# Optimization experiments

Hardware: AMD Instinct MI355X
Metric: run time of the kernel (lower is better)

The kernel has to match this reference:

```python
import jax, jax.numpy as jnp
import numpy as np
import math

N_EMBD = 768
N_HEAD = 12
B, T, S = 8, 1024, 257
HEAD_DIM = N_EMBD // N_HEAD


def _ln(x, g, b, eps=1e-5):
    m = jnp.mean(x, axis=-1, keepdims=True)
    v = jnp.mean(jnp.square(x - m), axis=-1, keepdims=True)
    return (x - m) * jax.lax.rsqrt(v + eps) * g + b


def _heads(t, n_head):
    b, s, c = t.shape
    return t.reshape(b, s, n_head, c // n_head).transpose(0, 2, 1, 3)  # (B,H,S,D)


def setup_inputs() -> dict:
    key = jax.random.key(0)
    ks = jax.random.split(key, 12)
    sc = 0.02
    d, h4 = N_EMBD, 4 * N_EMBD
    return {
        "x": jax.random.normal(ks[0], (B, T, d), jnp.float32),
        "encoder_x": jax.random.normal(ks[1], (B, S, d), jnp.float32),
        "ln1_g": jnp.ones((d,), jnp.float32), "ln1_b": jnp.zeros((d,), jnp.float32),
        "ln2_g": jnp.ones((d,), jnp.float32), "ln2_b": jnp.zeros((d,), jnp.float32),
        "ln3_g": jnp.ones((d,), jnp.float32), "ln3_b": jnp.zeros((d,), jnp.float32),
        "attn_w": jax.random.normal(ks[2], (d, 3 * d), jnp.float32) * sc,
        "attn_b": jnp.zeros((3 * d,), jnp.float32),
        "attn_proj_w": jax.random.normal(ks[3], (d, d), jnp.float32) * sc,
        "attn_proj_b": jnp.zeros((d,), jnp.float32),
        "cross_w": jax.random.normal(ks[4], (d, 3 * d), jnp.float32) * sc,
        "cross_b": jnp.zeros((3 * d,), jnp.float32),
        "cross_proj_w": jax.random.normal(ks[5], (d, d), jnp.float32) * sc,
        "cross_proj_b": jnp.zeros((d,), jnp.float32),
        "fc_w": jax.random.normal(ks[6], (d, h4), jnp.float32) * sc,
        "fc_b": jnp.zeros((h4,), jnp.float32),
        "proj_w": jax.random.normal(ks[7], (h4, d), jnp.float32) * sc,
        "proj_b": jnp.zeros((d,), jnp.float32),
    }


def reference(x, encoder_x, ln1_g, ln1_b, ln2_g, ln2_b, ln3_g, ln3_b,
              attn_w, attn_b, attn_proj_w, attn_proj_b,
              cross_w, cross_b, cross_proj_w, cross_proj_b,
              fc_w, fc_b, proj_w, proj_b):
    d = N_EMBD
    scale = 1.0 / math.sqrt(HEAD_DIM)

    # --- causal self-attention ---
    h = _ln(x, ln1_g, ln1_b)
    qkv = h @ attn_w + attn_b
    q, k, v = (_heads(t, N_HEAD) for t in jnp.split(qkv, 3, axis=-1))
    att = jnp.einsum('bhqd,bhkd->bhqk', q, k) * scale
    t = x.shape[1]
    causal = jnp.tril(jnp.ones((t, t), bool))
    att = jnp.where(causal[None, None], att, -jnp.inf)
    att = jax.nn.softmax(att, axis=-1)
    o = jnp.einsum('bhqk,bhkd->bhqd', att, v)
    o = o.transpose(0, 2, 1, 3).reshape(x.shape)
    x = x + o @ attn_proj_w + attn_proj_b

    # --- cross-attention (shared c_attn for q from x, k/v from encoder) ---
    h = _ln(x, ln2_g, ln2_b)
    q = _heads((h @ cross_w + cross_b)[..., :d], N_HEAD)
    ekv = encoder_x @ cross_w + cross_b
    k = _heads(ekv[..., d:2 * d], N_HEAD)
    v = _heads(ekv[..., 2 * d:], N_HEAD)
    att = jax.nn.softmax(jnp.einsum('bhqd,bhkd->bhqk', q, k) * scale, axis=-1)
    o = jnp.einsum('bhqk,bhkd->bhqd', att, v)
    o = o.transpose(0, 2, 1, 3).reshape(x.shape)
    x = x + o @ cross_proj_w + cross_proj_b

    # --- MLP (GELU tanh) ---
    h = _ln(x, ln3_g, ln3_b)
    h = jax.nn.gelu(h @ fc_w + fc_b, approximate=True)
    x = x + h @ proj_w + proj_b
    return x
```

## Files before the change

### kernel.cpp

```cpp
#include <hip/hip_runtime.h>

typedef __bf16 bf16x8 __attribute__((ext_vector_type(8)));
typedef float  f32x4  __attribute__((ext_vector_type(4)));
typedef unsigned short u16;

#define N_EMBD 768
#define T_LEN 1024
#define S_LEN 257
#define S_PAD 320
#define BATCH 8
#define NH 12
#define BH (BATCH*NH)
#define HD 64

__device__ __forceinline__ u16 f2b(float f){
  union{float f; unsigned u;} v; v.f=f;
  unsigned r=(v.u + 0x7fffu + ((v.u>>16)&1u))>>16;
  return (u16)r;
}
__device__ __forceinline__ float b2f(u16 h){
  union{unsigned u; float f;} v; v.u=((unsigned)h)<<16;
  return v.f;
}
__device__ __forceinline__ void gl_lds16(const void* g, void* l){
  __builtin_amdgcn_global_load_lds((const __attribute__((address_space(1))) void*)g,
                                   (__attribute__((address_space(3))) void*)l, 16, 0, 0);
}

template<int C> __device__ __forceinline__ float dpp_mov_f(float x){
  union{float f;int i;} u; u.f=x;
  u.i = __builtin_amdgcn_mov_dpp(u.i, C, 0xf, 0xf, true);
  return u.f;
}
__device__ __forceinline__ float red16_add(float x){
  x = x + dpp_mov_f<0xB1>(x);
  x = x + dpp_mov_f<0x4E>(x);
  x = x + dpp_mov_f<0x141>(x);
  x = x + dpp_mov_f<0x140>(x);
  return x;
}

__global__ void prep_all(const float* __restrict__ s0,const float* __restrict__ s1,
                         const float* __restrict__ s2,const float* __restrict__ s3,
                         const float* __restrict__ s4,const float* __restrict__ s5,
                         u16* __restrict__ d0,u16* __restrict__ d1,
                         u16* __restrict__ d2,u16* __restrict__ d3,
                         u16* __restrict__ d4,u16* __restrict__ d5,
                         const float* __restrict__ enc, u16* __restrict__ enc_bf,
                         const float* __restrict__ xin, const float* __restrict__ g1,
                         const float* __restrict__ b1, u16* __restrict__ hbuf){
  __shared__ u16 tile[64][68];
  int id=blockIdx.x;
  if(id>=3846){
    int row  = (id-3846)*4 + (threadIdx.x>>6);
    int lane = threadIdx.x&63;
    size_t base = (size_t)row*N_EMBD;
    float v[12];
#pragma unroll
    for(int p=0;p<3;p++){
      int col = p*256 + lane*4;
      float4 f = *(const float4*)&xin[base+col];
      v[p*4]=f.x; v[p*4+1]=f.y; v[p*4+2]=f.z; v[p*4+3]=f.w;
    }
    float s=0.f, s2=0.f;
#pragma unroll
    for(int i=0;i<12;i++){ s+=v[i]; s2+=v[i]*v[i]; }
#pragma unroll
    for(int off=1; off<64; off<<=1){ s += __shfl_xor(s,off); s2 += __shfl_xor(s2,off); }
    float mean = s*(1.f/N_EMBD);
    float var  = s2*(1.f/N_EMBD) - mean*mean;
    float rstd = rsqrtf(var + 1e-5f);
#pragma unroll
    for(int p=0;p<3;p++){
      int col = p*256 + lane*4;
#pragma unroll
      for(int j=0;j<4;j++){
        hbuf[base+col+j] = f2b((v[p*4+j]-mean)*rstd*g1[col+j] + b1[col+j]);
      }
    }
    return;
  }
  if(id>=2304){
    int i = (id-2304)*256 + threadIdx.x;
    float4 f = *(const float4*)&enc[i*4];
    ushort4 u; u.x=f2b(f.x); u.y=f2b(f.y); u.z=f2b(f.z); u.w=f2b(f.w);
    *(ushort4*)&enc_bf[i*4] = u;
    return;
  }
  const float* in; u16* out; int K,N,t;
  if(id<432)      {in=s0;out=d0;K=768;N=2304;t=id;}
  else if(id<864) {in=s1;out=d1;K=768;N=2304;t=id-432;}
  else if(id<1008){in=s2;out=d2;K=768;N=768;t=id-864;}
  else if(id<1152){in=s3;out=d3;K=768;N=768;t=id-1008;}
  else if(id<1728){in=s4;out=d4;K=768;N=3072;t=id-1152;}
  else            {in=s5;out=d5;K=3072;N=768;t=id-1728;}
  int tiles_n=N>>6;
  int k0=(t/tiles_n)<<6, n0=(t%tiles_n)<<6;
  int tr = threadIdx.x>>4;
  int tc = (threadIdx.x&15)*4;
#pragma unroll
  for(int i=0;i<4;i++){
    float4 f = *(const float4*)&in[(size_t)(k0+tr+i*16)*N + n0 + tc];
    tile[tr+i*16][tc+0]=f2b(f.x); tile[tr+i*16][tc+1]=f2b(f.y);
    tile[tr+i*16][tc+2]=f2b(f.z); tile[tr+i*16][tc+3]=f2b(f.w);
  }
  __syncthreads();
#pragma unroll
  for(int i=0;i<4;i++){
    int n = n0+tr+i*16;
    ushort4 u;
    u.x=tile[tc+0][tr+i*16]; u.y=tile[tc+1][tr+i*16];
    u.z=tile[tc+2][tr+i*16]; u.w=tile[tc+3][tr+i*16];
    *(ushort4*)&out[(size_t)n*K + k0 + tc] = u;
  }
}

__global__ void ln_kernel(const float* __restrict__ x, const float* __restrict__ g,
                          const float* __restrict__ bta, u16* __restrict__ out){
  int row  = blockIdx.x*4 + (threadIdx.x>>6);
  int lane = threadIdx.x&63;
  size_t base = (size_t)row*N_EMBD;
  float v[12];
#pragma unroll
  for(int p=0;p<3;p++){
    int col = p*256 + lane*4;
    float4 f = *(const float4*)&x[base+col];
    v[p*4]=f.x; v[p*4+1]=f.y; v[p*4+2]=f.z; v[p*4+3]=f.w;
  }
  float s=0.f, s2=0.f;
#pragma unroll
  for(int i=0;i<12;i++){ s+=v[i]; s2+=v[i]*v[i]; }
#pragma unroll
  for(int off=1; off<64; off<<=1){ s += __shfl_xor(s,off); s2 += __shfl_xor(s2,off); }
  float mean = s*(1.f/N_EMBD);
  float var  = s2*(1.f/N_EMBD) - mean*mean;
  float rstd = rsqrtf(var + 1e-5f);
#pragma unroll
  for(int p=0;p<3;p++){
    int col = p*256 + lane*4;
#pragma unroll
    for(int j=0;j<4;j++){
      out[base+col+j] = f2b((v[p*4+j]-mean)*rstd*g[col+j] + bta[col+j]);
    }
  }
}

enum { M_QKV_SELF=0, M_Q_CROSS=1, M_KV_CROSS=2, M_RESID_F32=3,
       M_RESID_INPLACE=4, M_GELU=5, M_RESID_OUT=6 };

template<int MODE, int BN>
__global__ void gemm_bt(const u16* __restrict__ A, const u16* __restrict__ Wt,
                        const float* __restrict__ bias,
                        void* out0, void* out1, void* out2, const void* resid,
                        int M, int K, int Ntiles){
  constexpr int MI = (BN==128)?4:2;
  __shared__ u16 As[128*64];
  __shared__ u16 Bs[BN*64];
  int tid=threadIdx.x, wave=tid>>6, lane=tid&63;

  int Mtl = gridDim.x / Ntiles;
  int mt, nt;
  if((Mtl&7)==0){
    int xcd=blockIdx.x&7, j=blockIdx.x>>3, bpx=Mtl>>3;
    int band=j/Ntiles; nt=j-band*Ntiles; mt=xcd*bpx+band;
  } else { mt=blockIdx.x/Ntiles; nt=blockIdx.x-mt*Ntiles; }
  int m0=mt*128, n0=nt*BN;

  int wm = (BN==128)? (wave>>1)*64 : wave*32;
  int wn = (BN==128)? (wave&1)*64  : 0;
  int lrow=lane&15, quad=lane>>4;
  f32x4 acc[MI][4];
  f32x4 z = {0.f,0.f,0.f,0.f};
#pragma unroll
  for(int i=0;i<MI;i++)
#pragma unroll
    for(int j=0;j<4;j++) acc[i][j]=z;

  int srow  = wave*8 + (lane>>3);
  int c_src = (lane&7) ^ ((lane>>3)&7);
  int pa = quad ^ (lrow&7);

  const u16* ap[4];
#pragma unroll
  for(int i=0;i<4;i++){
    int ga = min(m0 + i*32 + srow, M-1);
    ap[i] = A + (size_t)ga*K + c_src*8;
  }
  const u16* bp[BN/32];
#pragma unroll
  for(int i=0;i<BN/32;i++)
    bp[i] = Wt + (size_t)(n0 + i*32 + srow)*K + c_src*8;

  for(int k0=0;k0<K;k0+=64){
#pragma unroll
    for(int i=0;i<4;i++)
      gl_lds16(ap[i] + k0, &As[(i*32+wave*8)*64]);
#pragma unroll
    for(int i=0;i<BN/32;i++)
      gl_lds16(bp[i] + k0, &Bs[(i*32+wave*8)*64]);
    __syncthreads();
    bf16x8 af[MI][2], bfr[4][2];
#pragma unroll
    for(int i=0;i<MI;i++){
      const u16* ab=&As[(wm+i*16+lrow)*64];
      af[i][0]=*(const bf16x8*)(ab+pa*8);
      af[i][1]=*(const bf16x8*)(ab+(pa^4)*8);
    }
#pragma unroll
    for(int i=0;i<4;i++){
      const u16* bb=&Bs[(wn+i*16+lrow)*64];
      bfr[i][0]=*(const bf16x8*)(bb+pa*8);
      bfr[i][1]=*(const bf16x8*)(bb+(pa^4)*8);
    }
#pragma unroll
    for(int h=0;h<2;h++)
#pragma unroll
      for(int mi=0;mi<MI;mi++)
#pragma unroll
        for(int ni=0;ni<4;ni++)
          acc[mi][ni] = __builtin_amdgcn_mfma_f32_16x16x32_bf16(af[mi][h], bfr[ni][h], acc[mi][ni], 0,0,0);
    __syncthreads();
  }

#pragma unroll
  for(int ni=0;ni<4;ni++){
    int n = n0 + wn + ni*16 + lrow;
    float bv = bias[n];
#pragma unroll
    for(int mi=0;mi<MI;mi++){
      int mbase = m0 + wm + mi*16 + quad*4;
      float cr[4];
#pragma unroll
      for(int r=0;r<4;r++) cr[r]=acc[mi][ni][r]+bv;

      if constexpr (MODE==M_QKV_SELF){
        int part=n/768, nn=n-part*768;
        int hh=nn>>6, dd=nn&63;
        int b=mbase>>10, t0=mbase&1023;
        size_t bh=(size_t)(b*NH+hh);
        if(part==0){
#pragma unroll
          for(int r=0;r<4;r++) ((u16*)out0)[(bh*T_LEN+t0+r)*HD+dd]=f2b(cr[r]*0.125f);
        } else if(part==1){
#pragma unroll
          for(int r=0;r<4;r++) ((u16*)out1)[(bh*T_LEN+t0+r)*HD+dd]=f2b(cr[r]);
        } else {
          ushort4 pk; pk.x=f2b(cr[0]); pk.y=f2b(cr[1]); pk.z=f2b(cr[2]); pk.w=f2b(cr[3]);
          *(ushort4*)&((u16*)out2)[(bh*HD+dd)*T_LEN+t0]=pk;
        }
      } else if constexpr (MODE==M_Q_CROSS){
        int b=mbase>>10, t0=mbase&1023;
        int hh=n>>6, dd=n&63;
        size_t bh=(size_t)(b*NH+hh);
#pragma unroll
        for(int r=0;r<4;r++) ((u16*)out0)[(bh*T_LEN+t0+r)*HD+dd]=f2b(cr[r]*0.125f);
      } else if constexpr (MODE==M_KV_CROSS){
        int part=n/768, nn=n-part*768;
        int hh=nn>>6, dd=nn&63;
#pragma unroll
        for(int r=0;r<4;r++){
          int m=mbase+r;
          if(m<M){
            int b=m/S_LEN, s=m-b*S_LEN;
            size_t bh=(size_t)(b*NH+hh);
            if(part==0) ((u16*)out0)[(bh*S_PAD+s)*HD+dd]=f2b(cr[r]);
            else        ((u16*)out1)[(bh*HD+dd)*S_PAD+s]=f2b(cr[r]);
          }
        }
      } else if constexpr (MODE==M_RESID_F32){
        const float* x=(const float*)resid;
#pragma unroll
        for(int r=0;r<4;r++){ int m=mbase+r;
          ((float*)out0)[(size_t)m*768+n]=x[(size_t)m*768+n]+cr[r]; }
      } else if constexpr (MODE==M_RESID_INPLACE){
#pragma unroll
        for(int r=0;r<4;r++){ int m=mbase+r;
          ((float*)out0)[(size_t)m*768+n]+=cr[r]; }
      } else if constexpr (MODE==M_GELU){
#pragma unroll
        for(int r=0;r<4;r++){
          int m=mbase+r;
          float uu=cr[r];
          float zz=0.7978845608028654f*(uu+0.044715f*uu*uu*uu);
          float t=__expf(2.f*zz);
          float th=1.f-2.f/(t+1.f);
          ((u16*)out0)[(size_t)m*3072+n]=f2b(0.5f*uu*(1.f+th));
        }
      } else {
        const float* x=(const float*)resid;
#pragma unroll
        for(int r=0;r<4;r++){ int m=mbase+r;
          ((float*)out0)[(size_t)m*768+n]=x[(size_t)m*768+n]+cr[r]; }
      }
    }
  }
}

template<bool CAUSAL>
__global__ __launch_bounds__(256,2)
void flash_attn(const u16* __restrict__ Q, const u16* __restrict__ Kk,
                const u16* __restrict__ V, u16* __restrict__ O,
                int Skey, int Spad){
  __shared__ u16 KT[2][64*64];
  __shared__ u16 VT[2][64*64];
  __shared__ u16 Plds[4][16][72];
  int bh = blockIdx.x % BH;
  int qbi= blockIdx.x / BH;
  int qb = CAUSAL ? (15-qbi) : qbi;
  int b=bh/NH, hh=bh-b*NH;
  int wave=threadIdx.x>>6, lane=threadIdx.x&63;
  int lrow=lane&15, quad=lane>>4;
  const u16* Qp=Q+(size_t)bh*T_LEN*HD;
  const u16* Kp=Kk+(size_t)bh*Spad*HD;
  const u16* Vp=V+(size_t)bh*HD*Spad;
  u16* Op=O+(size_t)b*T_LEN*N_EMBD+hh*HD;
  int q0 = qb*64 + wave*16;

  int r0    = wave*8 + (lane>>3);
  int c_src = (lane&7) ^ ((lane>>3)&7);

  bf16x8 aq0=*(const bf16x8*)&Qp[(size_t)(q0+lrow)*HD + quad*8];
  bf16x8 aq1=*(const bf16x8*)&Qp[(size_t)(q0+lrow)*HD + 32 + quad*8];

  f32x4 oacc[4];
  f32x4 z={0.f,0.f,0.f,0.f};
#pragma unroll
  for(int i=0;i<4;i++) oacc[i]=z;
  float lsum[4]={0.f,0.f,0.f,0.f};

  int nt = CAUSAL ? (qb+1) : ((Skey+63)>>6);

  {
    gl_lds16(Kp + (size_t)r0*HD        + c_src*8, &KT[0][(wave*8)*64]);
    gl_lds16(Kp + (size_t)(r0+32)*HD   + c_src*8, &KT[0][(32+wave*8)*64]);
    gl_lds16(Vp + (size_t)r0*Spad      + c_src*8, &VT[0][(wave*8)*64]);
    gl_lds16(Vp + (size_t)(r0+32)*Spad + c_src*8, &VT[0][(32+wave*8)*64]);
  }
  __syncthreads();

  int p0 = quad ^ (lrow&7);

  for(int it=0; it<nt; it++){
    int bb = it&1;
    int kt = it*64;
    if(it+1<nt){
      int ktn=(it+1)*64;
      gl_lds16(Kp + (size_t)(ktn+r0)*HD      + c_src*8, &KT[bb^1][(wave*8)*64]);
      gl_lds16(Kp + (size_t)(ktn+r0+32)*HD   + c_src*8, &KT[bb^1][(32+wave*8)*64]);
      gl_lds16(Vp + (size_t)r0*Spad      + ktn + c_src*8, &VT[bb^1][(wave*8)*64]);
      gl_lds16(Vp + (size_t)(r0+32)*Spad + ktn + c_src*8, &VT[bb^1][(32+wave*8)*64]);
    }
    f32x4 s[4];
#pragma unroll
    for(int g=0;g<4;g++){
      const u16* kb=&KT[bb][(g*16+lrow)*64];
      bf16x8 bk0=*(const bf16x8*)(kb+p0*8);
      bf16x8 bk1=*(const bf16x8*)(kb+(p0^4)*8);
      s[g]=z;
      s[g]=__builtin_amdgcn_mfma_f32_16x16x32_bf16(aq0,bk0,s[g],0,0,0);
      s[g]=__builtin_amdgcn_mfma_f32_16x16x32_bf16(aq1,bk1,s[g],0,0,0);
    }
    bool domask = (it==nt-1);
#pragma unroll
    for(int r=0;r<4;r++){
      float sv0=s[0][r], sv1=s[1][r], sv2=s[2][r], sv3=s[3][r];
      if(domask){
        if(CAUSAL){
          int q=q0+quad*4+r;
          if(kt+lrow    >q) sv0=-3.0e38f;
          if(kt+16+lrow >q) sv1=-3.0e38f;
          if(kt+32+lrow >q) sv2=-3.0e38f;
          if(kt+48+lrow >q) sv3=-3.0e38f;
        } else {
          if(kt+lrow    >=Skey) sv0=-3.0e38f;
          if(kt+16+lrow >=Skey) sv1=-3.0e38f;
          if(kt+32+lrow >=Skey) sv2=-3.0e38f;
          if(kt+48+lrow >=Skey) sv3=-3.0e38f;
        }
      }
      float p0e=__expf(sv0), p1e=__expf(sv1);
      float p2e=__expf(sv2), p3e=__expf(sv3);
      lsum[r] += (p0e+p1e)+(p2e+p3e);
      Plds[wave][quad*4+r][lrow]    = f2b(p0e);
      Plds[wave][quad*4+r][16+lrow] = f2b(p1e);
      Plds[wave][quad*4+r][32+lrow] = f2b(p2e);
      Plds[wave][quad*4+r][48+lrow] = f2b(p3e);
    }
    bf16x8 ap0=*(const bf16x8*)&Plds[wave][lrow][quad*8];
    bf16x8 ap1=*(const bf16x8*)&Plds[wave][lrow][32+quad*8];
#pragma unroll
    for(int dt=0;dt<4;dt++){
      const u16* vb=&VT[bb][(dt*16+lrow)*64];
      bf16x8 bv0=*(const bf16x8*)(vb+p0*8);
      bf16x8 bv1=*(const bf16x8*)(vb+(p0^4)*8);
      oacc[dt]=__builtin_amdgcn_mfma_f32_16x16x32_bf16(ap0,bv0,oacc[dt],0,0,0);
      oacc[dt]=__builtin_amdgcn_mfma_f32_16x16x32_bf16(ap1,bv1,oacc[dt],0,0,0);
    }
    __syncthreads();
  }
  float linv[4];
#pragma unroll
  for(int r=0;r<4;r++) linv[r]=1.f/red16_add(lsum[r]);
#pragma unroll
  for(int dt=0;dt<4;dt++){
#pragma unroll
    for(int r=0;r<4;r++){
      int q=q0+quad*4+r;
      Op[(size_t)q*N_EMBD + dt*16 + lrow]=f2b(oacc[dt][r]*linv[r]);
    }
  }
}

extern "C" void kernel_launch(void* const* d_in, const int* in_sizes, int n_in,
                              void* d_out, int out_size, void* d_ws, size_t ws_size,
                              hipStream_t stream){
  const float* x_in   =(const float*)d_in[0];
  const float* enc    =(const float*)d_in[1];
  const float* ln1_g  =(const float*)d_in[2];
  const float* ln1_b  =(const float*)d_in[3];
  const float* ln2_g  =(const float*)d_in[4];
  const float* ln2_b  =(const float*)d_in[5];
  const float* ln3_g  =(const float*)d_in[6];
  const float* ln3_b  =(const float*)d_in[7];
  const float* attn_w =(const float*)d_in[8];
  const float* attn_b =(const float*)d_in[9];
  const float* attn_pw=(const float*)d_in[10];
  const float* attn_pb=(const float*)d_in[11];
  const float* cross_w=(const float*)d_in[12];
  const float* cross_b=(const float*)d_in[13];
  const float* cross_pw=(const float*)d_in[14];
  const float* cross_pb=(const float*)d_in[15];
  const float* fc_w   =(const float*)d_in[16];
  const float* fc_b   =(const float*)d_in[17];
  const float* proj_w =(const float*)d_in[18];
  const float* proj_b =(const float*)d_in[19];

  char* ws=(char*)d_ws;
  u16*  attn_wT  =(u16*)(ws + 0);
  u16*  cross_wT =(u16*)(ws + 3538944);
  u16*  attn_pwT =(u16*)(ws + 7077888);
  u16*  cross_pwT=(u16*)(ws + 8257536);
  u16*  fc_wT    =(u16*)(ws + 9437184);
  u16*  proj_wT  =(u16*)(ws + 14155776);
  float* xcur    =(float*)(ws + 18874368);
  u16*  hbuf     =(u16*)(ws + 44040192);
  u16*  Qs       =(u16*)(ws + 56623104);
  u16*  Ks       =(u16*)(ws + 69206016);
  u16*  Vst      =(u16*)(ws + 81788928);
  u16*  Qc       =(u16*)(ws + 94371840);
  u16*  hf       =(u16*)(ws + 56623104);
  u16*  Kc       =(u16*)(ws + 106954752);
  u16*  Vct      =(u16*)(ws + 110886912);
  u16*  enc_bf   =(u16*)(ws + 114819072);

  dim3 blk(256);
  prep_all<<<5894,blk,0,stream>>>(attn_w, cross_w, attn_pw, cross_pw, fc_w, proj_w,
                                  attn_wT, cross_wT, attn_pwT, cross_pwT, fc_wT, proj_wT,
                                  enc, enc_bf, x_in, ln1_g, ln1_b, hbuf);

  gemm_bt<M_QKV_SELF,128><<<1152,blk,0,stream>>>(hbuf, attn_wT, attn_b,
      Qs, Ks, Vst, nullptr, 8192, 768, 18);
  flash_attn<true><<<1536,blk,0,stream>>>(Qs, Ks, Vst, hbuf, 1024, 1024);
  gemm_bt<M_RESID_F32,64><<<768,blk,0,stream>>>(hbuf, attn_pwT, attn_pb,
      xcur, nullptr, nullptr, x_in, 8192, 768, 12);

  ln_kernel<<<2048,blk,0,stream>>>(xcur, ln2_g, ln2_b, hbuf);
  gemm_bt<M_Q_CROSS,64><<<768,blk,0,stream>>>(hbuf, cross_wT, cross_b,
      Qc, nullptr, nullptr, nullptr, 8192, 768, 12);
  gemm_bt<M_KV_CROSS,64><<<408,blk,0,stream>>>(enc_bf, cross_wT + 768*768,
      cross_b + 768, Kc, Vct, nullptr, nullptr, 2056, 768, 24);
  flash_attn<false><<<1536,blk,0,stream>>>(Qc, Kc, Vct, hbuf, S_LEN, S_PAD);
  gemm_bt<M_RESID_INPLACE,64><<<768,blk,0,stream>>>(hbuf, cross_pwT, cross_pb,
      xcur, nullptr, nullptr, nullptr, 8192, 768, 12);

  ln_kernel<<<2048,blk,0,stream>>>(xcur, ln3_g, ln3_b, hbuf);
  gemm_bt<M_GELU,128><<<1536,blk,0,stream>>>(hbuf, fc_wT, fc_b,
      hf, nullptr, nullptr, nullptr, 8192, 768, 24);
  gemm_bt<M_RESID_OUT,64><<<768,blk,0,stream>>>(hf, proj_wT, proj_b,
      d_out, nullptr, nullptr, xcur, 8192, 3072, 12);
}
```

Measured before the change: 441.2 us.

## Fold Q scale into weights, merge cross GEMMs, use hardware bf16 convert

New measurement: 424.9 us. 1.04x faster.

```diff
diff --git a/kernel.cpp b/kernel.cpp
--- a/kernel.cpp
+++ b/kernel.cpp
@@ -14,9 +14,7 @@
 #define HD 64
 
 __device__ __forceinline__ u16 f2b(float f){
-  union{float f; unsigned u;} v; v.f=f;
-  unsigned r=(v.u + 0x7fffu + ((v.u>>16)&1u))>>16;
-  return (u16)r;
+  union{ __bf16 h; u16 u; } v; v.h=(__bf16)f; return v.u;
 }
 __device__ __forceinline__ float b2f(u16 h){
   union{unsigned u; float f;} v; v.u=((unsigned)h)<<16;
@@ -48,9 +46,17 @@
                          u16* __restrict__ d4,u16* __restrict__ d5,
                          const float* __restrict__ enc, u16* __restrict__ enc_bf,
                          const float* __restrict__ xin, const float* __restrict__ g1,
-                         const float* __restrict__ b1, u16* __restrict__ hbuf){
+                         const float* __restrict__ b1, u16* __restrict__ hbuf,
+                         const float* __restrict__ attn_b, const float* __restrict__ cross_b,
+                         float* __restrict__ sb_attn, float* __restrict__ sb_cross){
   __shared__ u16 tile[64][68];
   int id=blockIdx.x;
+  if(id>=5894){
+    int i=(id-5894)*256+threadIdx.x;
+    if(i<2304)      sb_attn[i]       = attn_b[i]       *((i     <768)?0.125f:1.f);
+    else if(i<4608) sb_cross[i-2304] = cross_b[i-2304] *((i-2304<768)?0.125f:1.f);
+    return;
+  }
   if(id>=3846){
     int row  = (id-3846)*4 + (threadIdx.x>>6);
     int lane = threadIdx.x&63;
@@ -96,13 +102,14 @@
   else            {in=s5;out=d5;K=3072;N=768;t=id-1728;}
   int tiles_n=N>>6;
   int k0=(t/tiles_n)<<6, n0=(t%tiles_n)<<6;
+  float qs = (id<864 && n0<768) ? 0.125f : 1.f;
   int tr = threadIdx.x>>4;
   int tc = (threadIdx.x&15)*4;
 #pragma unroll
   for(int i=0;i<4;i++){
     float4 f = *(const float4*)&in[(size_t)(k0+tr+i*16)*N + n0 + tc];
-    tile[tr+i*16][tc+0]=f2b(f.x); tile[tr+i*16][tc+1]=f2b(f.y);
-    tile[tr+i*16][tc+2]=f2b(f.z); tile[tr+i*16][tc+3]=f2b(f.w);
+    tile[tr+i*16][tc+0]=f2b(f.x*qs); tile[tr+i*16][tc+1]=f2b(f.y*qs);
+    tile[tr+i*16][tc+2]=f2b(f.z*qs); tile[tr+i*16][tc+3]=f2b(f.w*qs);
   }
   __syncthreads();
 #pragma unroll
@@ -149,21 +156,19 @@
        M_RESID_INPLACE=4, M_GELU=5, M_RESID_OUT=6 };
 
 template<int MODE, int BN>
-__global__ void gemm_bt(const u16* __restrict__ A, const u16* __restrict__ Wt,
+__device__ __forceinline__ void gemm_body(u16* __restrict__ As, u16* __restrict__ Bs,
+                        const u16* __restrict__ A, const u16* __restrict__ Wt,
                         const float* __restrict__ bias,
                         void* out0, void* out1, void* out2, const void* resid,
-                        int M, int K, int Ntiles){
+                        int M, int K, int Ntiles, int Mtl, int bid){
   constexpr int MI = (BN==128)?4:2;
-  __shared__ u16 As[128*64];
-  __shared__ u16 Bs[BN*64];
   int tid=threadIdx.x, wave=tid>>6, lane=tid&63;
 
-  int Mtl = gridDim.x / Ntiles;
   int mt, nt;
   if((Mtl&7)==0){
-    int xcd=blockIdx.x&7, j=blockIdx.x>>3, bpx=Mtl>>3;
+    int xcd=bid&7, j=bid>>3, bpx=Mtl>>3;
     int band=j/Ntiles; nt=j-band*Ntiles; mt=xcd*bpx+band;
-  } else { mt=blockIdx.x/Ntiles; nt=blockIdx.x-mt*Ntiles; }
+  } else { mt=bid/Ntiles; nt=bid-mt*Ntiles; }
   int m0=mt*128, n0=nt*BN;
 
   int wm = (BN==128)? (wave>>1)*64 : wave*32;
@@ -240,7 +245,7 @@
         size_t bh=(size_t)(b*NH+hh);
         if(part==0){
 #pragma unroll
-          for(int r=0;r<4;r++) ((u16*)out0)[(bh*T_LEN+t0+r)*HD+dd]=f2b(cr[r]*0.125f);
+          for(int r=0;r<4;r++) ((u16*)out0)[(bh*T_LEN+t0+r)*HD+dd]=f2b(cr[r]);
         } else if(part==1){
 #pragma unroll
           for(int r=0;r<4;r++) ((u16*)out1)[(bh*T_LEN+t0+r)*HD+dd]=f2b(cr[r]);
@@ -253,7 +258,7 @@
         int hh=n>>6, dd=n&63;
         size_t bh=(size_t)(b*NH+hh);
 #pragma unroll
-        for(int r=0;r<4;r++) ((u16*)out0)[(bh*T_LEN+t0+r)*HD+dd]=f2b(cr[r]*0.125f);
+        for(int r=0;r<4;r++) ((u16*)out0)[(bh*T_LEN+t0+r)*HD+dd]=f2b(cr[r]);
       } else if constexpr (MODE==M_KV_CROSS){
         int part=n/768, nn=n-part*768;
         int hh=nn>>6, dd=nn&63;
@@ -282,9 +287,8 @@
           int m=mbase+r;
           float uu=cr[r];
           float zz=0.7978845608028654f*(uu+0.044715f*uu*uu*uu);
-          float t=__expf(2.f*zz);
-          float th=1.f-2.f/(t+1.f);
-          ((u16*)out0)[(size_t)m*3072+n]=f2b(0.5f*uu*(1.f+th));
+          float e=__expf(fminf(2.f*zz, 80.f));
+          ((u16*)out0)[(size_t)m*3072+n]=f2b(uu*e*__builtin_amdgcn_rcpf(e+1.f));
         }
       } else {
         const float* x=(const float*)resid;
@@ -294,6 +298,32 @@
       }
     }
   }
+}
+
+template<int MODE, int BN>
+__global__ __launch_bounds__(256,3)
+void gemm_bt(const u16* __restrict__ A, const u16* __restrict__ Wt,
+             const float* __restrict__ bias,
+             void* out0, void* out1, void* out2, const void* resid,
+             int M, int K, int Ntiles){
+  __shared__ u16 As[128*64];
+  __shared__ u16 Bs[BN*64];
+  gemm_body<MODE,BN>(As,Bs,A,Wt,bias,out0,out1,out2,resid,M,K,Ntiles,
+                     gridDim.x/Ntiles, blockIdx.x);
+}
+
+__global__ __launch_bounds__(256,3)
+void gemm_cross(const u16* __restrict__ hbuf, const u16* __restrict__ cwT,
+                const float* __restrict__ sbc, const u16* __restrict__ encbf,
+                void* Qc, void* Kc, void* Vct){
+  __shared__ u16 As[128*64];
+  __shared__ u16 Bs[64*64];
+  if(blockIdx.x<768)
+    gemm_body<M_Q_CROSS,64>(As,Bs,hbuf,cwT,sbc,Qc,nullptr,nullptr,nullptr,
+                            8192,768,12, 64, blockIdx.x);
+  else
+    gemm_body<M_KV_CROSS,64>(As,Bs,encbf,cwT+768*768,sbc+768,Kc,Vct,nullptr,nullptr,
+                             2056,768,24, 17, blockIdx.x-768);
 }
 
 template<bool CAUSAL>
@@ -452,23 +482,23 @@
   u16*  Kc       =(u16*)(ws + 106954752);
   u16*  Vct      =(u16*)(ws + 110886912);
   u16*  enc_bf   =(u16*)(ws + 114819072);
+  float* sb_attn =(float*)(ws + 117977088);
+  float* sb_cross=(float*)(ws + 117986304);
 
   dim3 blk(256);
-  prep_all<<<5894,blk,0,stream>>>(attn_w, cross_w, attn_pw, cross_pw, fc_w, proj_w,
+  prep_all<<<5912,blk,0,stream>>>(attn_w, cross_w, attn_pw, cross_pw, fc_w, proj_w,
                                   attn_wT, cross_wT, attn_pwT, cross_pwT, fc_wT, proj_wT,
-                                  enc, enc_bf, x_in, ln1_g, ln1_b, hbuf);
-
-  gemm_bt<M_QKV_SELF,128><<<1152,blk,0,stream>>>(hbuf, attn_wT, attn_b,
+                                  enc, enc_bf, x_in, ln1_g, ln1_b, hbuf,
+                                  attn_b, cross_b, sb_attn, sb_cross);
+
+  gemm_bt<M_QKV_SELF,128><<<1152,blk,0,stream>>>(hbuf, attn_wT, sb_attn,
       Qs, Ks, Vst, nullptr, 8192, 768, 18);
   flash_attn<true><<<1536,blk,0,stream>>>(Qs, Ks, Vst, hbuf, 1024, 1024);
   gemm_bt<M_RESID_F32,64><<<768,blk,0,stream>>>(hbuf, attn_pwT, attn_pb,
       xcur, nullptr, nullptr, x_in, 8192, 768, 12);
 
   ln_kernel<<<2048,blk,0,stream>>>(xcur, ln2_g, ln2_b, hbuf);
-  gemm_bt<M_Q_CROSS,64><<<768,blk,0,stream>>>(hbuf, cross_wT, cross_b,
-      Qc, nullptr, nullptr, nullptr, 8192, 768, 12);
-  gemm_bt<M_KV_CROSS,64><<<408,blk,0,stream>>>(enc_bf, cross_wT + 768*768,
-      cross_b + 768, Kc, Vct, nullptr, nullptr, 2056, 768, 24);
+  gemm_cross<<<1176,blk,0,stream>>>(hbuf, cross_wT, sb_cross, enc_bf, Qc, Kc, Vct);
   flash_attn<false><<<1536,blk,0,stream>>>(Qc, Kc, Vct, hbuf, S_LEN, S_PAD);
   gemm_bt<M_RESID_INPLACE,64><<<768,blk,0,stream>>>(hbuf, cross_pwT, cross_pb,
       xcur, nullptr, nullptr, nullptr, 8192, 768, 12);
```
